# Kernel tuning notes

Measured on AMD Instinct MI355X. Metric: run time of the kernel, lower is better.

Reference implementation:

```python
import jax, jax.numpy as jnp
import numpy as np

NEG_INF = -1.0e9  # matches the source's close_to_negative_inf


def setup_inputs() -> dict:
    key = jax.random.key(0)
    k1, k2, k3, k4 = jax.random.split(key, 4)
    B, S, H, Dh = 2, 2048, 16, 64
    d_model = H * Dh
    return {
        "pre_q": jax.random.normal(k1, (B, S, H, Dh), dtype=jnp.float32),
        "pre_v": jax.random.normal(k2, (B, S, H, Dh), dtype=jnp.float32),
        "pre_k": jax.random.normal(k3, (B, S, H, Dh), dtype=jnp.float32),
        "output_weights": jax.random.normal(k4, (d_model, d_model), dtype=jnp.float32) * (1.0 / np.sqrt(d_model)),
        "out_seq_len": S,
        "d_model": d_model,
    }


def reference(pre_q, pre_v, pre_k, output_weights, out_seq_len, d_model):
    B, S, H, Dh = pre_q.shape
    # (B, H, S, Dh)
    q = jnp.transpose(pre_q, (0, 2, 1, 3))
    k = jnp.transpose(pre_k, (0, 2, 1, 3))
    v = jnp.transpose(pre_v, (0, 2, 1, 3))
    scale = 1.0 / jnp.sqrt(jnp.float32(Dh))
    # scaled QK^T: (B, H, Sq, Sk)
    scores = jnp.einsum("bhqd,bhkd->bhqk", q, k) * scale
    # source masking: multiply by lower triangle, add -1e9 on upper triangle
    tril = jnp.tril(jnp.ones((S, S), dtype=scores.dtype))
    masked = tril * scores + NEG_INF * (1.0 - tril)
    attn = jax.nn.softmax(masked, axis=-1)
    heads = jnp.einsum("bhqk,bhkd->bhqd", attn, v)  # (B, H, S, Dh)
    merged = jnp.transpose(heads, (0, 2, 1, 3)).reshape(B, S, H * Dh)
    out = jnp.einsum("bsd,de->bse", merged, output_weights)
    return out.reshape(-1, out_seq_len, d_model)
```

## Files before the change

### kernel.cpp

```cpp
#include <hip/hip_runtime.h>
#include <stdint.h>

#define S_LEN 2048
#define NH 16
#define DH 64
#define DM 1024

typedef __attribute__((ext_vector_type(8))) short short8;
typedef __attribute__((ext_vector_type(4))) float f32x4;

__device__ __forceinline__ unsigned short f2bf(float f) {
  union { float f; uint32_t u; } c; c.f = f;
  uint32_t u = c.u;
  return (unsigned short)((u + 0x7FFFu + ((u >> 16) & 1u)) >> 16);
}

__device__ __forceinline__ uint32_t pk_bf16(float lo, float hi) {
  uint32_t r;
  asm("v_cvt_pk_bf16_f32 %0, %1, %2" : "=v"(r) : "v"(lo), "v"(hi));
  return r;
}

__device__ __forceinline__ void g2l16(const void* g, void* l) {
  __builtin_amdgcn_global_load_lds(
      (const __attribute__((address_space(1))) uint32_t*)g,
      (__attribute__((address_space(3))) uint32_t*)l, 16, 0, 0);
}

__global__ __launch_bounds__(256) void wtrans_kernel(const float* __restrict__ W,
                                                     unsigned short* __restrict__ Wt) {
  __shared__ __align__(16) unsigned short tile[64 * 72];
  const int tid = threadIdx.x;
  const int e0 = blockIdx.x << 6;
  const int d0 = blockIdx.y << 6;
#pragma unroll
  for (int i = 0; i < 4; ++i) {
    int idx = tid + i * 256;
    int d = idx >> 4;
    int ec = (idx & 15) << 2;
    float4 w = *(const float4*)(W + (size_t)(d0 + d) * DM + e0 + ec);
    tile[(ec + 0) * 72 + d] = f2bf(w.x);
    tile[(ec + 1) * 72 + d] = f2bf(w.y);
    tile[(ec + 2) * 72 + d] = f2bf(w.z);
    tile[(ec + 3) * 72 + d] = f2bf(w.w);
  }
  __syncthreads();
#pragma unroll
  for (int i = 0; i < 2; ++i) {
    int idx = tid + i * 256;
    int e = idx >> 3;
    int g = idx & 7;
    uint4 v = *(const uint4*)&tile[e * 72 + (g << 3)];
    *(uint4*)(Wt + (size_t)(e0 + e) * DM + d0 + ((g ^ (e & 7)) << 3)) = v;
  }
}

__global__ __launch_bounds__(256) void prep_kernel(const float* __restrict__ K,
                                                   const float* __restrict__ V,
                                                   unsigned short* __restrict__ Kb,
                                                   unsigned short* __restrict__ Vt) {
  __shared__ __align__(16) unsigned short tile[64 * 72];
  const int tid = threadIdx.x;
  const int blk = blockIdx.x;
  const int st = blk & 31;
  const int bh = blk >> 5;
  const int b = bh >> 4;
  const int h = bh & 15;
  const int s0 = st << 6;
  const size_t ibase = (size_t)b * (S_LEN * DM) + (size_t)h * DH;
  const size_t kbase = (size_t)bh * (S_LEN * DH);
  const size_t vbase = (size_t)bh * (DH * S_LEN);

#pragma unroll
  for (int i = 0; i < 4; ++i) {
    int idx = tid + i * 256;
    int s = idx >> 4;
    int d4 = (idx & 15) << 2;
    int g = d4 >> 3, rem = d4 & 7;
    float4 kv = *(const float4*)(K + ibase + (size_t)(s0 + s) * DM + d4);
    uint2 u;
    u.x = pk_bf16(kv.x, kv.y);
    u.y = pk_bf16(kv.z, kv.w);
    *(uint2*)(Kb + kbase + (size_t)(s0 + s) * DH + ((g ^ (s & 7)) << 3) + rem) = u;
  }
#pragma unroll
  for (int i = 0; i < 4; ++i) {
    int idx = tid + i * 256;
    int s = idx >> 4;
    int d4 = (idx & 15) << 2;
    float4 vv = *(const float4*)(V + ibase + (size_t)(s0 + s) * DM + d4);
    tile[(d4 + 0) * 72 + s] = f2bf(vv.x);
    tile[(d4 + 1) * 72 + s] = f2bf(vv.y);
    tile[(d4 + 2) * 72 + s] = f2bf(vv.z);
    tile[(d4 + 3) * 72 + s] = f2bf(vv.w);
  }
  __syncthreads();
#pragma unroll
  for (int i = 0; i < 2; ++i) {
    int idx = tid + i * 256;
    int d = idx >> 3;
    int g = idx & 7;
    uint4 u = *(const uint4*)&tile[d * 72 + (g << 3)];
    *(uint4*)(Vt + vbase + (size_t)d * S_LEN + s0 + ((g ^ (d & 7)) << 3)) = u;
  }
}

__global__ __launch_bounds__(256) void attn_kernel(const float* __restrict__ Q,
                                                   const unsigned short* __restrict__ Kb,
                                                   const unsigned short* __restrict__ Vt,
                                                   unsigned short* __restrict__ merged) {
  __shared__ __align__(16) unsigned short kbuf[2][64 * 64];
  __shared__ __align__(16) unsigned short vbuf[2][64 * 64];
  __shared__ __align__(16) unsigned short p_lds[4 * 16 * 72];

  const int tid = threadIdx.x;
  const int wave = tid >> 6;
  const int lane = tid & 63;
  const int t = lane & 15;
  const int qd = lane >> 4;
  const int tx = t & 7;

  const int bid = blockIdx.x;
  const int qt = 31 - (bid >> 5);
  const int bh = bid & 31;
  const int h = bh & 15;
  const int b = bh >> 4;

  const int q0 = qt << 6;
  const int row0 = q0 + (wave << 4);
  const size_t qbase = (size_t)b * (S_LEN * DM) + (size_t)h * DH;
  const size_t kbase = (size_t)bh * (S_LEN * DH);
  const size_t vbase = (size_t)bh * (DH * S_LEN);
  const unsigned short* kg = Kb + kbase;
  const unsigned short* vg = Vt + vbase;

  short8 qfrag[2];
  {
    const float SC = 0.125f * 1.4426950408889634f;
    const float* qp = Q + qbase + (size_t)(row0 + t) * DM + (qd << 3);
#pragma unroll
    for (int kk = 0; kk < 2; ++kk) {
      float4 f0 = *(const float4*)(qp + kk * 32);
      float4 f1 = *(const float4*)(qp + kk * 32 + 4);
      union { short8 s; uint32_t u[4]; } qq;
      qq.u[0] = pk_bf16(f0.x * SC, f0.y * SC);
      qq.u[1] = pk_bf16(f0.z * SC, f0.w * SC);
      qq.u[2] = pk_bf16(f1.x * SC, f1.y * SC);
      qq.u[3] = pk_bf16(f1.z * SC, f1.w * SC);
      qfrag[kk] = qq.s;
    }
  }

  const int c1 = wave * 512;
  const int c2 = (wave + 4) * 512;
  const int l8 = lane * 8;
  auto stage = [&](int bsel, int kt0) {
    g2l16(kg + (size_t)kt0 * DH + c1 + l8, &kbuf[bsel][c1]);
    g2l16(kg + (size_t)kt0 * DH + c2 + l8, &kbuf[bsel][c2]);
    int o1 = c1 + l8, o2 = c2 + l8;
    g2l16(vg + (size_t)(o1 >> 6) * S_LEN + kt0 + (o1 & 63), &vbuf[bsel][c1]);
    g2l16(vg + (size_t)(o2 >> 6) * S_LEN + kt0 + (o2 & 63), &vbuf[bsel][c2]);
  };

  const f32x4 fzero = {0.f, 0.f, 0.f, 0.f};
  float lsum = 0.f;
  f32x4 o_acc[4];
#pragma unroll
  for (int nb = 0; nb < 4; ++nb) o_acc[nb] = fzero;

  unsigned short* pw = &p_lds[wave * (16 * 72)];

  const int ntiles = qt + 1;
  stage(0, 0);
  asm volatile("s_waitcnt vmcnt(0)" ::: "memory");
  __syncthreads();
  int cur = 0;

  for (int tile = 0; tile < ntiles; ++tile) {
    const int kt0 = tile << 6;
    if (tile + 1 < ntiles) stage(cur ^ 1, (tile + 1) << 6);

    const unsigned short* kl = kbuf[cur];
    const unsigned short* vl = vbuf[cur];

    f32x4 sc[4];
#pragma unroll
    for (int cb = 0; cb < 4; ++cb) {
      const int row = cb * 16 + t;
      short8 a0 = *(const short8*)&kl[row * 64 + ((qd ^ tx) << 3)];
      short8 a1 = *(const short8*)&kl[row * 64 + (((4 | qd) ^ tx) << 3)];
      f32x4 a = fzero;
      a = __builtin_amdgcn_mfma_f32_16x16x32_bf16(a0, qfrag[0], a, 0, 0, 0);
      a = __builtin_amdgcn_mfma_f32_16x16x32_bf16(a1, qfrag[1], a, 0, 0, 0);
      sc[cb] = a;
    }

    if (tile == ntiles - 1) {
#pragma unroll
      for (int cb = 0; cb < 4; ++cb)
#pragma unroll
        for (int r = 0; r < 4; ++r)
          if (kt0 + cb * 16 + qd * 4 + r > row0 + t) sc[cb][r] = -INFINITY;
    }

#pragma unroll
    for (int cb = 0; cb < 4; ++cb)
#pragma unroll
      for (int r = 0; r < 4; ++r)
        sc[cb][r] = __builtin_amdgcn_exp2f(sc[cb][r]);
    lsum += ((sc[0][0] + sc[0][1]) + (sc[0][2] + sc[0][3])) +
            ((sc[1][0] + sc[1][1]) + (sc[1][2] + sc[1][3])) +
            ((sc[2][0] + sc[2][1]) + (sc[2][2] + sc[2][3])) +
            ((sc[3][0] + sc[3][1]) + (sc[3][2] + sc[3][3]));

#pragma unroll
    for (int cb = 0; cb < 4; ++cb) {
      uint2 u;
      u.x = pk_bf16(sc[cb][0], sc[cb][1]);
      u.y = pk_bf16(sc[cb][2], sc[cb][3]);
      *(uint2*)&pw[t * 72 + cb * 16 + qd * 4] = u;
    }
    asm volatile("s_waitcnt lgkmcnt(0)" ::: "memory");

#pragma unroll
    for (int kk = 0; kk < 2; ++kk) {
      short8 pa = *(const short8*)&pw[t * 72 + kk * 32 + (qd << 3)];
#pragma unroll
      for (int nb = 0; nb < 4; ++nb) {
        short8 vfr = *(const short8*)&vl[(nb * 16 + t) * 64 + (((4 * kk + qd) ^ tx) << 3)];
        o_acc[nb] = __builtin_amdgcn_mfma_f32_16x16x32_bf16(vfr, pa, o_acc[nb], 0, 0, 0);
      }
    }

    asm volatile("s_waitcnt vmcnt(0)" ::: "memory");
    __syncthreads();
    cur ^= 1;
  }

  lsum += __shfl_xor(lsum, 16);
  lsum += __shfl_xor(lsum, 32);
  const float invl = __builtin_amdgcn_rcpf(lsum);

#pragma unroll
  for (int nb = 0; nb < 4; ++nb) {
    uint2 u;
    u.x = pk_bf16(o_acc[nb][0] * invl, o_acc[nb][1] * invl);
    u.y = pk_bf16(o_acc[nb][2] * invl, o_acc[nb][3] * invl);
    *(uint2*)&pw[t * 72 + nb * 16 + qd * 4] = u;
  }
  asm volatile("s_waitcnt lgkmcnt(0)" ::: "memory");
  {
    uint4 u0 = *(const uint4*)&pw[t * 72 + qd * 16];
    uint4 u1 = *(const uint4*)&pw[t * 72 + qd * 16 + 8];
    unsigned short* mp = merged + (size_t)(b * S_LEN + row0 + t) * DM + h * DH;
    *(uint4*)(mp + (((2 * qd) ^ tx) << 3)) = u0;
    *(uint4*)(mp + (((2 * qd + 1) ^ tx) << 3)) = u1;
  }
}

__global__ __launch_bounds__(256) void gemm_kernel(const unsigned short* __restrict__ A,
                                                   const unsigned short* __restrict__ Bt,
                                                   float* __restrict__ C) {
  __shared__ __align__(16) unsigned short abuf[2][128 * 64];
  __shared__ __align__(16) unsigned short bbuf[2][128 * 64];
  const int tid = threadIdx.x;
  const int wave = tid >> 6;
  const int lane = tid & 63;
  const int t = lane & 15;
  const int qd = lane >> 4;
  const int tx = t & 7;
  const int wm = wave >> 1;
  const int wn = wave & 1;
  const int n0 = blockIdx.x << 7;
  const int m0 = blockIdx.y << 7;

  const int rin = lane >> 3;
  const int cin = (lane & 7) << 3;
  auto stage = [&](int bsel, int kt) {
#pragma unroll
    for (int i = 0; i < 4; ++i) {
      int c = wave * 4 + i;
      int row = c * 8 + rin;
      g2l16(A + (size_t)(m0 + row) * DM + kt + cin, &abuf[bsel][c * 512]);
      g2l16(Bt + (size_t)(n0 + row) * DM + kt + cin, &bbuf[bsel][c * 512]);
    }
  };

  const f32x4 fzero = {0.f, 0.f, 0.f, 0.f};
  f32x4 acc[4][4];
#pragma unroll
  for (int mi = 0; mi < 4; ++mi)
#pragma unroll
    for (int nb = 0; nb < 4; ++nb) acc[mi][nb] = fzero;

  stage(0, 0);
  asm volatile("s_waitcnt vmcnt(0)" ::: "memory");
  __syncthreads();
  int cur = 0;

  for (int kt = 0; kt < DM; kt += 64) {
    if (kt + 64 < DM) stage(cur ^ 1, kt + 64);
    const unsigned short* al = abuf[cur];
    const unsigned short* bl = bbuf[cur];
#pragma unroll
    for (int kk = 0; kk < 2; ++kk) {
      const int sw = ((kk * 4 + qd) ^ tx) << 3;
      short8 af[4], bf[4];
#pragma unroll
      for (int mi = 0; mi < 4; ++mi)
        af[mi] = *(const short8*)&al[(wm * 64 + mi * 16 + t) * 64 + sw];
#pragma unroll
      for (int nb = 0; nb < 4; ++nb)
        bf[nb] = *(const short8*)&bl[(wn * 64 + nb * 16 + t) * 64 + sw];
#pragma unroll
      for (int mi = 0; mi < 4; ++mi)
#pragma unroll
        for (int nb = 0; nb < 4; ++nb)
          acc[mi][nb] = __builtin_amdgcn_mfma_f32_16x16x32_bf16(af[mi], bf[nb], acc[mi][nb], 0, 0, 0);
    }
    asm volatile("s_waitcnt vmcnt(0)" ::: "memory");
    __syncthreads();
    cur ^= 1;
  }
#pragma unroll
  for (int mi = 0; mi < 4; ++mi)
#pragma unroll
    for (int nb = 0; nb < 4; ++nb)
#pragma unroll
      for (int r = 0; r < 4; ++r)
        C[(size_t)(m0 + wm * 64 + mi * 16 + qd * 4 + r) * DM + n0 + wn * 64 + nb * 16 + t] =
            acc[mi][nb][r];
}

extern "C" void kernel_launch(void* const* d_in, const int* in_sizes, int n_in,
                              void* d_out, int out_size, void* d_ws, size_t ws_size,
                              hipStream_t stream) {
  const float* pre_q = (const float*)d_in[0];
  const float* pre_v = (const float*)d_in[1];
  const float* pre_k = (const float*)d_in[2];
  const float* W     = (const float*)d_in[3];
  float* out = (float*)d_out;

  unsigned short* Wt = (unsigned short*)d_ws;
  unsigned short* merged = Wt + (size_t)DM * DM;
  unsigned short* Kb = merged + (size_t)4096 * DM;
  unsigned short* Vt = Kb + (size_t)32 * S_LEN * DH;

  wtrans_kernel<<<dim3(16, 16), 256, 0, stream>>>(W, Wt);
  prep_kernel<<<dim3(1024), 256, 0, stream>>>(pre_k, pre_v, Kb, Vt);
  attn_kernel<<<dim3(1024), 256, 0, stream>>>(pre_q, Kb, Vt, merged);
  gemm_kernel<<<dim3(8, 32), 256, 0, stream>>>(merged, Wt, out);
}
```

Baseline: 156.0 us.

## Merge weight transpose into prep kernel, triple-buffer attention, permlane P exchange

Folds the weight transpose into the K/V prep kernel as extra blocks, removing one launch. The attention kernel moves from double to triple buffering of K/V tiles with a single barrier per iteration and partial vmcnt waits. It also replaces the LDS round trip for the P matrix and the output with v_permlane32/16 swaps, freeing shared memory. The GEMM loop moves its wait and barrier to the top of the iteration. The permlane lane mapping has to match the MFMA operand layout exactly, and the extra buffer raises LDS use.

```diff
diff --git a/kernel.cpp b/kernel.cpp
--- a/kernel.cpp
+++ b/kernel.cpp
@@ -27,41 +27,46 @@
       (__attribute__((address_space(3))) uint32_t*)l, 16, 0, 0);
 }
 
-__global__ __launch_bounds__(256) void wtrans_kernel(const float* __restrict__ W,
-                                                     unsigned short* __restrict__ Wt) {
-  __shared__ __align__(16) unsigned short tile[64 * 72];
-  const int tid = threadIdx.x;
-  const int e0 = blockIdx.x << 6;
-  const int d0 = blockIdx.y << 6;
-#pragma unroll
-  for (int i = 0; i < 4; ++i) {
-    int idx = tid + i * 256;
-    int d = idx >> 4;
-    int ec = (idx & 15) << 2;
-    float4 w = *(const float4*)(W + (size_t)(d0 + d) * DM + e0 + ec);
-    tile[(ec + 0) * 72 + d] = f2bf(w.x);
-    tile[(ec + 1) * 72 + d] = f2bf(w.y);
-    tile[(ec + 2) * 72 + d] = f2bf(w.z);
-    tile[(ec + 3) * 72 + d] = f2bf(w.w);
-  }
-  __syncthreads();
-#pragma unroll
-  for (int i = 0; i < 2; ++i) {
-    int idx = tid + i * 256;
-    int e = idx >> 3;
-    int g = idx & 7;
-    uint4 v = *(const uint4*)&tile[e * 72 + (g << 3)];
-    *(uint4*)(Wt + (size_t)(e0 + e) * DM + d0 + ((g ^ (e & 7)) << 3)) = v;
-  }
-}
+#define PL32(a, b) asm("v_permlane32_swap_b32 %0, %1" : "+v"(a), "+v"(b))
+#define PL16(a, b) asm("v_permlane16_swap_b32 %0, %1" : "+v"(a), "+v"(b))
 
 __global__ __launch_bounds__(256) void prep_kernel(const float* __restrict__ K,
                                                    const float* __restrict__ V,
+                                                   const float* __restrict__ W,
                                                    unsigned short* __restrict__ Kb,
-                                                   unsigned short* __restrict__ Vt) {
+                                                   unsigned short* __restrict__ Vt,
+                                                   unsigned short* __restrict__ Wt) {
   __shared__ __align__(16) unsigned short tile[64 * 72];
   const int tid = threadIdx.x;
   const int blk = blockIdx.x;
+
+  if (blk >= 1024) {
+    const int wb = blk - 1024;
+    const int e0 = (wb & 15) << 6;
+    const int d0 = (wb >> 4) << 6;
+#pragma unroll
+    for (int i = 0; i < 4; ++i) {
+      int idx = tid + i * 256;
+      int d = idx >> 4;
+      int ec = (idx & 15) << 2;
+      float4 w = *(const float4*)(W + (size_t)(d0 + d) * DM + e0 + ec);
+      tile[(ec + 0) * 72 + d] = f2bf(w.x);
+      tile[(ec + 1) * 72 + d] = f2bf(w.y);
+      tile[(ec + 2) * 72 + d] = f2bf(w.z);
+      tile[(ec + 3) * 72 + d] = f2bf(w.w);
+    }
+    __syncthreads();
+#pragma unroll
+    for (int i = 0; i < 2; ++i) {
+      int idx = tid + i * 256;
+      int e = idx >> 3;
+      int g = idx & 7;
+      uint4 v = *(const uint4*)&tile[e * 72 + (g << 3)];
+      *(uint4*)(Wt + (size_t)(e0 + e) * DM + d0 + ((g ^ (e & 7)) << 3)) = v;
+    }
+    return;
+  }
+
   const int st = blk & 31;
   const int bh = blk >> 5;
   const int b = bh >> 4;
@@ -109,9 +114,8 @@
                                                    const unsigned short* __restrict__ Kb,
                                                    const unsigned short* __restrict__ Vt,
                                                    unsigned short* __restrict__ merged) {
-  __shared__ __align__(16) unsigned short kbuf[2][64 * 64];
-  __shared__ __align__(16) unsigned short vbuf[2][64 * 64];
-  __shared__ __align__(16) unsigned short p_lds[4 * 16 * 72];
+  __shared__ __align__(16) unsigned short kbuf[3][64 * 64];
+  __shared__ __align__(16) unsigned short vbuf[3][64 * 64];
 
   const int tid = threadIdx.x;
   const int wave = tid >> 6;
@@ -129,10 +133,8 @@
   const int q0 = qt << 6;
   const int row0 = q0 + (wave << 4);
   const size_t qbase = (size_t)b * (S_LEN * DM) + (size_t)h * DH;
-  const size_t kbase = (size_t)bh * (S_LEN * DH);
-  const size_t vbase = (size_t)bh * (DH * S_LEN);
-  const unsigned short* kg = Kb + kbase;
-  const unsigned short* vg = Vt + vbase;
+  const unsigned short* kg = Kb + (size_t)bh * (S_LEN * DH);
+  const unsigned short* vg = Vt + (size_t)bh * (DH * S_LEN);
 
   short8 qfrag[2];
   {
@@ -168,20 +170,22 @@
 #pragma unroll
   for (int nb = 0; nb < 4; ++nb) o_acc[nb] = fzero;
 
-  unsigned short* pw = &p_lds[wave * (16 * 72)];
-
   const int ntiles = qt + 1;
   stage(0, 0);
-  asm volatile("s_waitcnt vmcnt(0)" ::: "memory");
-  __syncthreads();
-  int cur = 0;
+  if (ntiles > 1) stage(1, 64);
+  int b0 = 0, b1 = 1, b2 = 2;
 
   for (int tile = 0; tile < ntiles; ++tile) {
-    const int kt0 = tile << 6;
-    if (tile + 1 < ntiles) stage(cur ^ 1, (tile + 1) << 6);
-
-    const unsigned short* kl = kbuf[cur];
-    const unsigned short* vl = vbuf[cur];
+    if (tile + 1 < ntiles)
+      asm volatile("s_waitcnt vmcnt(4)" ::: "memory");
+    else
+      asm volatile("s_waitcnt vmcnt(0)" ::: "memory");
+    __builtin_amdgcn_s_barrier();
+    asm volatile("" ::: "memory");
+    if (tile + 2 < ntiles) stage(b2, (tile + 2) << 6);
+
+    const unsigned short* kl = kbuf[b0];
+    const unsigned short* vl = vbuf[b0];
 
     f32x4 sc[4];
 #pragma unroll
@@ -200,7 +204,7 @@
       for (int cb = 0; cb < 4; ++cb)
 #pragma unroll
         for (int r = 0; r < 4; ++r)
-          if (kt0 + cb * 16 + qd * 4 + r > row0 + t) sc[cb][r] = -INFINITY;
+          if ((tile << 6) + cb * 16 + qd * 4 + r > row0 + t) sc[cb][r] = -INFINITY;
     }
 
 #pragma unroll
@@ -213,49 +217,55 @@
             ((sc[2][0] + sc[2][1]) + (sc[2][2] + sc[2][3])) +
             ((sc[3][0] + sc[3][1]) + (sc[3][2] + sc[3][3]));
 
-#pragma unroll
-    for (int cb = 0; cb < 4; ++cb) {
-      uint2 u;
-      u.x = pk_bf16(sc[cb][0], sc[cb][1]);
-      u.y = pk_bf16(sc[cb][2], sc[cb][3]);
-      *(uint2*)&pw[t * 72 + cb * 16 + qd * 4] = u;
-    }
-    asm volatile("s_waitcnt lgkmcnt(0)" ::: "memory");
-
-#pragma unroll
-    for (int kk = 0; kk < 2; ++kk) {
-      short8 pa = *(const short8*)&pw[t * 72 + kk * 32 + (qd << 3)];
-#pragma unroll
-      for (int nb = 0; nb < 4; ++nb) {
-        short8 vfr = *(const short8*)&vl[(nb * 16 + t) * 64 + (((4 * kk + qd) ^ tx) << 3)];
-        o_acc[nb] = __builtin_amdgcn_mfma_f32_16x16x32_bf16(vfr, pa, o_acc[nb], 0, 0, 0);
-      }
-    }
-
-    asm volatile("s_waitcnt vmcnt(0)" ::: "memory");
-    __syncthreads();
-    cur ^= 1;
+    uint32_t p00 = pk_bf16(sc[0][0], sc[0][1]);
+    uint32_t p01 = pk_bf16(sc[0][2], sc[0][3]);
+    uint32_t p10 = pk_bf16(sc[1][0], sc[1][1]);
+    uint32_t p11 = pk_bf16(sc[1][2], sc[1][3]);
+    uint32_t p20 = pk_bf16(sc[2][0], sc[2][1]);
+    uint32_t p21 = pk_bf16(sc[2][2], sc[2][3]);
+    uint32_t p30 = pk_bf16(sc[3][0], sc[3][1]);
+    uint32_t p31 = pk_bf16(sc[3][2], sc[3][3]);
+    PL32(p00, p10); PL32(p01, p11);
+    PL16(p00, p10); PL16(p01, p11);
+    PL32(p20, p30); PL32(p21, p31);
+    PL16(p20, p30); PL16(p21, p31);
+    union { short8 s; uint32_t u[4]; } pa0, pa1;
+    pa0.u[0] = p00; pa0.u[1] = p01; pa0.u[2] = p10; pa0.u[3] = p11;
+    pa1.u[0] = p20; pa1.u[1] = p21; pa1.u[2] = p30; pa1.u[3] = p31;
+
+#pragma unroll
+    for (int nb = 0; nb < 4; ++nb) {
+      short8 v0 = *(const short8*)&vl[(nb * 16 + t) * 64 + ((qd ^ tx) << 3)];
+      o_acc[nb] = __builtin_amdgcn_mfma_f32_16x16x32_bf16(v0, pa0.s, o_acc[nb], 0, 0, 0);
+      short8 v1 = *(const short8*)&vl[(nb * 16 + t) * 64 + (((4 | qd) ^ tx) << 3)];
+      o_acc[nb] = __builtin_amdgcn_mfma_f32_16x16x32_bf16(v1, pa1.s, o_acc[nb], 0, 0, 0);
+    }
+
+    int tb = b0; b0 = b1; b1 = b2; b2 = tb;
   }
 
   lsum += __shfl_xor(lsum, 16);
   lsum += __shfl_xor(lsum, 32);
   const float invl = __builtin_amdgcn_rcpf(lsum);
 
-#pragma unroll
-  for (int nb = 0; nb < 4; ++nb) {
-    uint2 u;
-    u.x = pk_bf16(o_acc[nb][0] * invl, o_acc[nb][1] * invl);
-    u.y = pk_bf16(o_acc[nb][2] * invl, o_acc[nb][3] * invl);
-    *(uint2*)&pw[t * 72 + nb * 16 + qd * 4] = u;
-  }
-  asm volatile("s_waitcnt lgkmcnt(0)" ::: "memory");
-  {
-    uint4 u0 = *(const uint4*)&pw[t * 72 + qd * 16];
-    uint4 u1 = *(const uint4*)&pw[t * 72 + qd * 16 + 8];
-    unsigned short* mp = merged + (size_t)(b * S_LEN + row0 + t) * DM + h * DH;
-    *(uint4*)(mp + (((2 * qd) ^ tx) << 3)) = u0;
-    *(uint4*)(mp + (((2 * qd + 1) ^ tx) << 3)) = u1;
-  }
+  uint32_t e00 = pk_bf16(o_acc[0][0] * invl, o_acc[0][1] * invl);
+  uint32_t e01 = pk_bf16(o_acc[0][2] * invl, o_acc[0][3] * invl);
+  uint32_t e10 = pk_bf16(o_acc[1][0] * invl, o_acc[1][1] * invl);
+  uint32_t e11 = pk_bf16(o_acc[1][2] * invl, o_acc[1][3] * invl);
+  uint32_t e20 = pk_bf16(o_acc[2][0] * invl, o_acc[2][1] * invl);
+  uint32_t e21 = pk_bf16(o_acc[2][2] * invl, o_acc[2][3] * invl);
+  uint32_t e30 = pk_bf16(o_acc[3][0] * invl, o_acc[3][1] * invl);
+  uint32_t e31 = pk_bf16(o_acc[3][2] * invl, o_acc[3][3] * invl);
+  PL32(e00, e20); PL32(e10, e30);
+  PL16(e00, e10); PL16(e20, e30);
+  PL32(e01, e21); PL32(e11, e31);
+  PL16(e01, e11); PL16(e21, e31);
+  union { uint4 v; uint32_t u[4]; } u0, u1;
+  u0.u[0] = e00; u0.u[1] = e01; u0.u[2] = e10; u0.u[3] = e11;
+  u1.u[0] = e20; u1.u[1] = e21; u1.u[2] = e30; u1.u[3] = e31;
+  unsigned short* mp = merged + (size_t)(b * S_LEN + row0 + t) * DM + h * DH;
+  *(uint4*)(mp + (((2 * qd) ^ tx) << 3)) = u0.v;
+  *(uint4*)(mp + (((2 * qd + 1) ^ tx) << 3)) = u1.v;
 }
 
 __global__ __launch_bounds__(256) void gemm_kernel(const unsigned short* __restrict__ A,
@@ -294,11 +304,12 @@
     for (int nb = 0; nb < 4; ++nb) acc[mi][nb] = fzero;
 
   stage(0, 0);
-  asm volatile("s_waitcnt vmcnt(0)" ::: "memory");
-  __syncthreads();
   int cur = 0;
 
   for (int kt = 0; kt < DM; kt += 64) {
+    asm volatile("s_waitcnt vmcnt(0)" ::: "memory");
+    __builtin_amdgcn_s_barrier();
+    asm volatile("" ::: "memory");
     if (kt + 64 < DM) stage(cur ^ 1, kt + 64);
     const unsigned short* al = abuf[cur];
     const unsigned short* bl = bbuf[cur];
@@ -318,8 +329,6 @@
         for (int nb = 0; nb < 4; ++nb)
           acc[mi][nb] = __builtin_amdgcn_mfma_f32_16x16x32_bf16(af[mi], bf[nb], acc[mi][nb], 0, 0, 0);
     }
-    asm volatile("s_waitcnt vmcnt(0)" ::: "memory");
-    __syncthreads();
     cur ^= 1;
   }
 #pragma unroll
@@ -346,8 +355,7 @@
   unsigned short* Kb = merged + (size_t)4096 * DM;
   unsigned short* Vt = Kb + (size_t)32 * S_LEN * DH;
 
-  wtrans_kernel<<<dim3(16, 16), 256, 0, stream>>>(W, Wt);
-  prep_kernel<<<dim3(1024), 256, 0, stream>>>(pre_k, pre_v, Kb, Vt);
+  prep_kernel<<<dim3(1280), 256, 0, stream>>>(pre_k, pre_v, W, Kb, Vt, Wt);
   attn_kernel<<<dim3(1024), 256, 0, stream>>>(pre_q, Kb, Vt, merged);
   gemm_kernel<<<dim3(8, 32), 256, 0, stream>>>(merged, Wt, out);
 }
```

Result: faster. 152.5 us (-2.2%).
